# Optimization experiments

Measured on AMD Instinct MI355X. Metric: run time of the kernel, lower is better.

Reference implementation:

```python
import jax, jax.numpy as jnp
import numpy as np

B, C, H, W = 16, 512, 32, 32
GROUPS = 8
EPS = 1e-5


def setup_inputs() -> dict:
    key = jax.random.key(0)
    ks = jax.random.split(key, 7)
    s = 1.0 / np.sqrt(C)
    return {
        "x": jax.random.normal(ks[0], (B, C, H, W), dtype=jnp.float32),
        "gamma": jnp.ones((C,), dtype=jnp.float32),
        "beta": jnp.zeros((C,), dtype=jnp.float32),
        "w_qkv": jax.random.normal(ks[1], (3 * C, C), dtype=jnp.float32) * s,
        "b_qkv": jnp.zeros((3 * C,), dtype=jnp.float32),
        "w_proj": jax.random.normal(ks[2], (C, C), dtype=jnp.float32) * s,
        "b_proj": jnp.zeros((C,), dtype=jnp.float32),
    }


def group_norm(x, gamma, beta):
    b, c, h, w = x.shape
    xg = x.reshape(b, GROUPS, c // GROUPS, h, w)
    mean = xg.mean(axis=(2, 3, 4), keepdims=True)
    var = xg.var(axis=(2, 3, 4), keepdims=True)
    xn = ((xg - mean) * jax.lax.rsqrt(var + EPS)).reshape(b, c, h, w)
    return xn * gamma[None, :, None, None] + beta[None, :, None, None]


def reference(x, gamma, beta, w_qkv, b_qkv, w_proj, b_proj):
    b, c, h, w = x.shape
    n = h * w
    hn = group_norm(x, gamma, beta)
    # 1x1 conv == channel matmul: [3C, C] x [B, C, N] -> [B, 3C, N]
    qkv = jnp.einsum('oc,bcn->bon', w_qkv, hn.reshape(b, c, n)) + b_qkv[None, :, None]
    q, k, v = jnp.split(qkv, 3, axis=1)  # each [B, C, N]
    scale = c ** (-0.5)
    # scores [B, N, N]: q^T k
    attn = jax.nn.softmax(jnp.einsum('bcn,bcm->bnm', q, k) * scale, axis=-1)
    out = jnp.einsum('bnm,bcm->bcn', attn, v)  # [B, C, N]
    proj = jnp.einsum('oc,bcn->bon', w_proj, out) + b_proj[None, :, None]
    return x + proj.reshape(b, c, h, w)
```

## Files before the change

kernel.cpp:

```cpp
#include <hip/hip_runtime.h>


#define BATCH 16
#define CCH 512
#define NSP 1024
#define EPSV 1e-5f
#define BK 32

typedef short bf16x8 __attribute__((ext_vector_type(8)));
typedef float f32x4 __attribute__((ext_vector_type(4)));

__device__ __forceinline__ unsigned short f2bf(float f) {
    unsigned int u = __float_as_uint(f);
    u += 0x7FFF + ((u >> 16) & 1);
    return (unsigned short)(u >> 16);
}

__device__ __forceinline__ void glds16(const void* g, void* l) {
    __builtin_amdgcn_global_load_lds(
        (const __attribute__((address_space(1))) unsigned int*)g,
        (__attribute__((address_space(3))) unsigned int*)l, 16, 0, 0);
}

#define XCD_MAP(GX_LOG2, PER, xv, yv, bv)                 \
    const int lin_ = blockIdx.x;                          \
    const int xcd_ = lin_ & 7;                            \
    int slot_ = lin_ >> 3;                                \
    const int hi_ = (slot_ >= (PER)) ? 1 : 0;             \
    const int bv = xcd_ + 8 * hi_;                        \
    slot_ -= hi_ * (PER);                                 \
    const int xv = slot_ & ((1 << (GX_LOG2)) - 1);        \
    const int yv = slot_ >> (GX_LOG2);

__device__ __forceinline__ void gemm128_loop(
    const unsigned short* __restrict__ Ag, const unsigned short* __restrict__ Bg,
    int astr, int bstr, int ktot, short* Al, short* Bl, f32x4* acc) {
    const int t = threadIdx.x;
    const int w = t >> 6, lane = t & 63;
    const int wr = (w >> 1) * 64, wc = (w & 1) * 64;
    const int fr = lane & 15, fko = (lane >> 4) * 8;
    const int r0 = t >> 2;
    const int kc = (t & 3) * 8;
    short* Alb0 = Al + w * 512;
    short* Alb1 = Al + 2048 + w * 512;
    short* Blb0 = Bl + w * 512;
    short* Blb1 = Bl + 2048 + w * 512;
    for (int k0 = 0; k0 < ktot; k0 += BK) {
        glds16(Ag + (size_t)r0 * astr + k0 + kc, Alb0);
        glds16(Ag + (size_t)(r0 + 64) * astr + k0 + kc, Alb1);
        glds16(Bg + (size_t)r0 * bstr + k0 + kc, Blb0);
        glds16(Bg + (size_t)(r0 + 64) * bstr + k0 + kc, Blb1);
        __syncthreads();
        bf16x8 af[4], bfr[4];
#pragma unroll
        for (int mi = 0; mi < 4; mi++)
            af[mi] = *(const bf16x8*)(Al + (wr + mi * 16 + fr) * BK + fko);
#pragma unroll
        for (int ni = 0; ni < 4; ni++)
            bfr[ni] = *(const bf16x8*)(Bl + (wc + ni * 16 + fr) * BK + fko);
#pragma unroll
        for (int mi = 0; mi < 4; mi++)
#pragma unroll
            for (int ni = 0; ni < 4; ni++)
                acc[mi * 4 + ni] = __builtin_amdgcn_mfma_f32_16x16x32_bf16(
                    af[mi], bfr[ni], acc[mi * 4 + ni], 0, 0, 0);
        __syncthreads();
    }
}

#define EPI_SETUP()                                          \
    const int t = threadIdx.x, lane = t & 63, w = t >> 6;    \
    const int wr = (w >> 1) * 64, wc = (w & 1) * 64;         \
    const int fr = lane & 15, rr0 = (lane >> 4) * 4;

#define ACC_INIT(acc)                                        \
    f32x4 acc[16];                                           \
    _Pragma("unroll") for (int i = 0; i < 16; i++)           \
        acc[i] = (f32x4){0.f, 0.f, 0.f, 0.f};

__global__ __launch_bounds__(256) void setup_k(
    const float* __restrict__ x, float* __restrict__ stats,
    const float* __restrict__ wa, unsigned short* __restrict__ oa, int na4,
    const float* __restrict__ wb, unsigned short* __restrict__ ob, int nb4) {
    const int t = threadIdx.x;
    if (blockIdx.x < 128) {
        const int bg = blockIdx.x;
        const float4* xp = (const float4*)(x + (size_t)bg * 65536);
        float s = 0.f, q = 0.f;
#pragma unroll
        for (int i = 0; i < 64; i++) {
            float4 v = xp[t + i * 256];
            s += v.x + v.y + v.z + v.w;
            q += v.x * v.x + v.y * v.y + v.z * v.z + v.w * v.w;
        }
#pragma unroll
        for (int off = 32; off; off >>= 1) {
            s += __shfl_down(s, off);
            q += __shfl_down(q, off);
        }
        __shared__ float rs[4], rq[4];
        const int wave = t >> 6, lane = t & 63;
        if (lane == 0) { rs[wave] = s; rq[wave] = q; }
        __syncthreads();
        if (t == 0) {
            float S = rs[0] + rs[1] + rs[2] + rs[3];
            float Q = rq[0] + rq[1] + rq[2] + rq[3];
            const float inv = 1.f / 65536.f;
            float mean = S * inv;
            float var = Q * inv - mean * mean;
            stats[bg * 2] = mean;
            stats[bg * 2 + 1] = rsqrtf(var + EPSV);
        }
    } else {
        int i = (blockIdx.x - 128) * 256 + t;
        const float* src;
        unsigned short* dst;
        int j;
        if (i < na4) { src = wa; dst = oa; j = i; }
        else { j = i - na4; if (j >= nb4) return; src = wb; dst = ob; }
        float4 v = ((const float4*)src)[j];
        ushort4 o;
        o.x = f2bf(v.x); o.y = f2bf(v.y); o.z = f2bf(v.z); o.w = f2bf(v.w);
        ((ushort4*)dst)[j] = o;
    }
}

__global__ __launch_bounds__(256) void gn_tr_k(
    const float* __restrict__ x, const float* __restrict__ gamma,
    const float* __restrict__ beta, const float* __restrict__ stats,
    unsigned short* __restrict__ hn_t) {
    const int nt = blockIdx.x, ct = blockIdx.y, b = blockIdx.z;
    __shared__ __align__(16) unsigned short T[64 * 72];
    const int t = threadIdx.x;
    const float mean = stats[(b * 8 + ct) * 2];
    const float rstd = stats[(b * 8 + ct) * 2 + 1];
    const int cl = t >> 2, nc = t & 3;
    const int c = ct * 64 + cl;
    const float ga = gamma[c] * rstd;
    const float be = beta[c] - mean * ga;
    const float4* xp = (const float4*)(x + ((size_t)b * CCH + c) * NSP + nt * 64);
#pragma unroll
    for (int j = 0; j < 4; j++) {
        float4 v = xp[nc * 4 + j];
        int n = nc * 16 + j * 4;
        T[(n + 0) * 72 + cl] = f2bf(v.x * ga + be);
        T[(n + 1) * 72 + cl] = f2bf(v.y * ga + be);
        T[(n + 2) * 72 + cl] = f2bf(v.z * ga + be);
        T[(n + 3) * 72 + cl] = f2bf(v.w * ga + be);
    }
    __syncthreads();
    const int nl = t >> 2, cc = t & 3;
    unsigned short* dst = hn_t + ((size_t)b * NSP + nt * 64 + nl) * CCH + ct * 64 + cc * 16;
    const unsigned short* src = T + nl * 72 + cc * 16;
    *(uint4*)dst = *(const uint4*)src;
    *(uint4*)(dst + 8) = *(const uint4*)(src + 8);
}

__global__ __launch_bounds__(256) void gemm_qkv_k(
    const unsigned short* __restrict__ hn_t, const unsigned short* __restrict__ wq,
    const float* __restrict__ bq, unsigned short* __restrict__ QKt,
    unsigned short* __restrict__ Vb) {
    __shared__ __align__(16) short Al[128 * BK], Bl[128 * BK];
    XCD_MAP(3, 96, xb, y, b);
    const int ntc = xb * 128;
    ACC_INIT(acc);
    if (y < 8) {
        const int mt = y * 128;
        gemm128_loop(hn_t + ((size_t)b * NSP + mt) * CCH,
                     wq + (size_t)ntc * CCH, CCH, CCH, CCH, Al, Bl, acc);
        unsigned short* Ob = QKt + (size_t)b * NSP * 1024;
        EPI_SETUP();
#pragma unroll
        for (int ni = 0; ni < 4; ni++) {
            int col = ntc + wc + ni * 16 + fr;
            float bias = bq[col];
#pragma unroll
            for (int mi = 0; mi < 4; mi++) {
                int row = mt + wr + mi * 16 + rr0;
#pragma unroll
                for (int r = 0; r < 4; r++)
                    Ob[(size_t)(row + r) * 1024 + col] = f2bf(acc[mi * 4 + ni][r] + bias);
            }
        }
    } else {
        const int mt = (y - 8) * 128;
        gemm128_loop(wq + (size_t)(1024 + mt) * CCH,
                     hn_t + ((size_t)b * NSP + ntc) * CCH, CCH, CCH, CCH, Al, Bl, acc);
        unsigned short* Ob = Vb + (size_t)b * CCH * NSP;
        EPI_SETUP();
#pragma unroll
        for (int mi = 0; mi < 4; mi++) {
            int row = mt + wr + mi * 16 + rr0;
#pragma unroll
            for (int r = 0; r < 4; r++) {
                float bias = bq[1024 + row + r];
#pragma unroll
                for (int ni = 0; ni < 4; ni++) {
                    int col = ntc + wc + ni * 16 + fr;
                    Ob[(size_t)(row + r) * NSP + col] = f2bf(acc[mi * 4 + ni][r] + bias);
                }
            }
        }
    }
}

__global__ __launch_bounds__(256) void gemm_scores_k(
    const unsigned short* __restrict__ QKt, unsigned short* __restrict__ expS,
    float* __restrict__ Lsum) {
    __shared__ __align__(16) short Al[128 * BK], Bl[128 * BK];
    XCD_MAP(3, 64, xb, yb, b);
    const int nt = xb * 128, mt = yb * 128;
    const unsigned short* base = QKt + (size_t)b * NSP * 1024;
    ACC_INIT(acc);
    gemm128_loop(base + (size_t)mt * 1024, base + (size_t)nt * 1024 + 512,
                 1024, 1024, 512, Al, Bl, acc);
    unsigned short* Ob = expS + (size_t)b * NSP * NSP;
    float* Ls = Lsum + (size_t)b * NSP;
    const float scale = 0.044194173824159216f;
    EPI_SETUP();
#pragma unroll
    for (int mi = 0; mi < 4; mi++) {
#pragma unroll
        for (int r = 0; r < 4; r++) {
            const int row = mt + wr + mi * 16 + rr0 + r;
            float rs = 0.f;
#pragma unroll
            for (int ni = 0; ni < 4; ni++) {
                int col = nt + wc + ni * 16 + fr;
                float e = __expf(acc[mi * 4 + ni][r] * scale);
                Ob[(size_t)row * NSP + col] = f2bf(e);
                rs += e;
            }
            rs += __shfl_xor(rs, 1);
            rs += __shfl_xor(rs, 2);
            rs += __shfl_xor(rs, 4);
            rs += __shfl_xor(rs, 8);
            if (fr == 0) atomicAdd(&Ls[row], rs);
        }
    }
}

__global__ __launch_bounds__(256) void gemm_pv_k(
    const unsigned short* __restrict__ expS, const unsigned short* __restrict__ Vb,
    const float* __restrict__ Lsum, unsigned short* __restrict__ At) {
    __shared__ __align__(16) short Al[128 * BK], Bl[128 * BK];
    XCD_MAP(2, 32, xb, yb, b);
    const int ntc = xb * 128, mt = yb * 128;
    ACC_INIT(acc);
    gemm128_loop(expS + ((size_t)b * NSP + mt) * NSP,
                 Vb + ((size_t)b * CCH + ntc) * NSP, NSP, NSP, NSP, Al, Bl, acc);
    unsigned short* Ob = At + (size_t)b * NSP * CCH;
    const float* Ls = Lsum + (size_t)b * NSP;
    EPI_SETUP();
#pragma unroll
    for (int mi = 0; mi < 4; mi++) {
        int row = mt + wr + mi * 16 + rr0;
#pragma unroll
        for (int r = 0; r < 4; r++) {
            float inv = __builtin_amdgcn_rcpf(Ls[row + r]);
#pragma unroll
            for (int ni = 0; ni < 4; ni++) {
                int col = ntc + wc + ni * 16 + fr;
                Ob[(size_t)(row + r) * CCH + col] = f2bf(acc[mi * 4 + ni][r] * inv);
            }
        }
    }
}

__global__ __launch_bounds__(256) void gemm_proj_k(
    const unsigned short* __restrict__ At, const unsigned short* __restrict__ wp,
    const float* __restrict__ bp, const float* __restrict__ x,
    float* __restrict__ out) {
    __shared__ __align__(16) short Al[128 * BK], Bl[128 * BK];
    XCD_MAP(3, 32, xb, yb, b);
    const int nt = xb * 128, mt = yb * 128;
    ACC_INIT(acc);
    gemm128_loop(wp + (size_t)mt * CCH, At + ((size_t)b * NSP + nt) * CCH,
                 CCH, CCH, CCH, Al, Bl, acc);
    const size_t bbase = (size_t)b * CCH * NSP;
    EPI_SETUP();
#pragma unroll
    for (int mi = 0; mi < 4; mi++) {
        int row = mt + wr + mi * 16 + rr0;
#pragma unroll
        for (int r = 0; r < 4; r++) {
            float bias = bp[row + r];
#pragma unroll
            for (int ni = 0; ni < 4; ni++) {
                int col = nt + wc + ni * 16 + fr;
                size_t idx = bbase + (size_t)(row + r) * NSP + col;
                out[idx] = x[idx] + bias + acc[mi * 4 + ni][r];
            }
        }
    }
}

extern "C" void kernel_launch(void* const* d_in, const int* in_sizes, int n_in,
                              void* d_out, int out_size, void* d_ws, size_t ws_size,
                              hipStream_t stream) {
    const float* x = (const float*)d_in[0];
    const float* gamma = (const float*)d_in[1];
    const float* beta = (const float*)d_in[2];
    const float* w_qkv = (const float*)d_in[3];
    const float* b_qkv = (const float*)d_in[4];
    const float* w_proj = (const float*)d_in[5];
    const float* b_proj = (const float*)d_in[6];
    float* out = (float*)d_out;

    char* ws = (char*)d_ws;
    const size_t MB = 1048576;
    unsigned short* wqkv_bf = (unsigned short*)ws;
    unsigned short* wproj_bf = (unsigned short*)(ws + 1572864);
    float* stats = (float*)(ws + 2 * MB);
    float* Lsum = (float*)(ws + 2 * MB + 65536);
    unsigned short* hn_t = (unsigned short*)(ws + 4 * MB);
    unsigned short* At = hn_t;
    unsigned short* QKt = (unsigned short*)(ws + 24 * MB);
    unsigned short* Vb = (unsigned short*)(ws + 60 * MB);
    unsigned short* expS = (unsigned short*)(ws + 80 * MB);

    hipMemsetAsync(Lsum, 0, BATCH * NSP * sizeof(float), stream);
    setup_k<<<1152, 256, 0, stream>>>(x, stats, w_qkv, wqkv_bf, 196608,
                                      w_proj, wproj_bf, 65536);
    gn_tr_k<<<dim3(16, 8, BATCH), 256, 0, stream>>>(x, gamma, beta, stats, hn_t);
    gemm_qkv_k<<<1536, 256, 0, stream>>>(hn_t, wqkv_bf, b_qkv, QKt, Vb);
    gemm_scores_k<<<1024, 256, 0, stream>>>(QKt, expS, Lsum);
    gemm_pv_k<<<512, 256, 0, stream>>>(expS, Vb, Lsum, At);
    gemm_proj_k<<<512, 256, 0, stream>>>(At, wproj_bf, b_proj, x, out);
}
```

Before: 225.7 us.

## Double-buffer GEMM LDS tiles with register prefetch and fold Lsum memset into setup

Replaces the direct global-to-LDS loads in the shared GEMM loop with a register-staged, double-buffered pipeline. The next K tile is loaded into registers while MFMAs run on the current LDS buffer, then written to the other buffer, so each step needs one barrier instead of two. It also drops the separate hipMemsetAsync by zeroing Lsum in extra blocks of setup_k. The cost is double the LDS per block, which may lower occupancy, plus extra VGPRs and VALU/LDS store instructions compared with the direct-to-LDS loads.

```diff
diff --git a/kernel.cpp b/kernel.cpp
--- a/kernel.cpp
+++ b/kernel.cpp
@@ -6,6 +6,7 @@
 #define NSP 1024
 #define EPSV 1e-5f
 #define BK 32
+#define BUFSZ 4096
 
 typedef short bf16x8 __attribute__((ext_vector_type(8)));
 typedef float f32x4 __attribute__((ext_vector_type(4)));
@@ -14,12 +15,6 @@
     unsigned int u = __float_as_uint(f);
     u += 0x7FFF + ((u >> 16) & 1);
     return (unsigned short)(u >> 16);
-}
-
-__device__ __forceinline__ void glds16(const void* g, void* l) {
-    __builtin_amdgcn_global_load_lds(
-        (const __attribute__((address_space(1))) unsigned int*)g,
-        (__attribute__((address_space(3))) unsigned int*)l, 16, 0, 0);
 }
 
 #define XCD_MAP(GX_LOG2, PER, xv, yv, bv)                 \
@@ -41,31 +36,66 @@
     const int fr = lane & 15, fko = (lane >> 4) * 8;
     const int r0 = t >> 2;
     const int kc = (t & 3) * 8;
-    short* Alb0 = Al + w * 512;
-    short* Alb1 = Al + 2048 + w * 512;
-    short* Blb0 = Bl + w * 512;
-    short* Blb1 = Bl + 2048 + w * 512;
-    for (int k0 = 0; k0 < ktot; k0 += BK) {
-        glds16(Ag + (size_t)r0 * astr + k0 + kc, Alb0);
-        glds16(Ag + (size_t)(r0 + 64) * astr + k0 + kc, Alb1);
-        glds16(Bg + (size_t)r0 * bstr + k0 + kc, Blb0);
-        glds16(Bg + (size_t)(r0 + 64) * bstr + k0 + kc, Blb1);
-        __syncthreads();
+    const unsigned short* Ap0 = Ag + (size_t)r0 * astr + kc;
+    const unsigned short* Ap1 = Ag + (size_t)(r0 + 64) * astr + kc;
+    const unsigned short* Bp0 = Bg + (size_t)r0 * bstr + kc;
+    const unsigned short* Bp1 = Bg + (size_t)(r0 + 64) * bstr + kc;
+    const int wof0 = r0 * BK + kc;
+    const int wof1 = (r0 + 64) * BK + kc;
+    bf16x8 ra0 = *(const bf16x8*)Ap0;
+    bf16x8 ra1 = *(const bf16x8*)Ap1;
+    bf16x8 rb0 = *(const bf16x8*)Bp0;
+    bf16x8 rb1 = *(const bf16x8*)Bp1;
+    *(bf16x8*)(Al + wof0) = ra0;
+    *(bf16x8*)(Al + wof1) = ra1;
+    *(bf16x8*)(Bl + wof0) = rb0;
+    *(bf16x8*)(Bl + wof1) = rb1;
+    __syncthreads();
+    const int nk = ktot / BK;
+    int buf = 0;
+    for (int k = 0; k < nk - 1; k++) {
+        const int kof = (k + 1) * BK;
+        ra0 = *(const bf16x8*)(Ap0 + kof);
+        ra1 = *(const bf16x8*)(Ap1 + kof);
+        rb0 = *(const bf16x8*)(Bp0 + kof);
+        rb1 = *(const bf16x8*)(Bp1 + kof);
+        const short* Ab = Al + buf * BUFSZ;
+        const short* Bb = Bl + buf * BUFSZ;
         bf16x8 af[4], bfr[4];
 #pragma unroll
         for (int mi = 0; mi < 4; mi++)
-            af[mi] = *(const bf16x8*)(Al + (wr + mi * 16 + fr) * BK + fko);
+            af[mi] = *(const bf16x8*)(Ab + (wr + mi * 16 + fr) * BK + fko);
 #pragma unroll
         for (int ni = 0; ni < 4; ni++)
-            bfr[ni] = *(const bf16x8*)(Bl + (wc + ni * 16 + fr) * BK + fko);
+            bfr[ni] = *(const bf16x8*)(Bb + (wc + ni * 16 + fr) * BK + fko);
 #pragma unroll
         for (int mi = 0; mi < 4; mi++)
 #pragma unroll
             for (int ni = 0; ni < 4; ni++)
                 acc[mi * 4 + ni] = __builtin_amdgcn_mfma_f32_16x16x32_bf16(
                     af[mi], bfr[ni], acc[mi * 4 + ni], 0, 0, 0);
+        buf ^= 1;
+        *(bf16x8*)(Al + buf * BUFSZ + wof0) = ra0;
+        *(bf16x8*)(Al + buf * BUFSZ + wof1) = ra1;
+        *(bf16x8*)(Bl + buf * BUFSZ + wof0) = rb0;
+        *(bf16x8*)(Bl + buf * BUFSZ + wof1) = rb1;
         __syncthreads();
     }
+    const short* Ab = Al + buf * BUFSZ;
+    const short* Bb = Bl + buf * BUFSZ;
+    bf16x8 af[4], bfr[4];
+#pragma unroll
+    for (int mi = 0; mi < 4; mi++)
+        af[mi] = *(const bf16x8*)(Ab + (wr + mi * 16 + fr) * BK + fko);
+#pragma unroll
+    for (int ni = 0; ni < 4; ni++)
+        bfr[ni] = *(const bf16x8*)(Bb + (wc + ni * 16 + fr) * BK + fko);
+#pragma unroll
+    for (int mi = 0; mi < 4; mi++)
+#pragma unroll
+        for (int ni = 0; ni < 4; ni++)
+            acc[mi * 4 + ni] = __builtin_amdgcn_mfma_f32_16x16x32_bf16(
+                af[mi], bfr[ni], acc[mi * 4 + ni], 0, 0, 0);
 }
 
 #define EPI_SETUP()                                          \
@@ -81,7 +111,8 @@
 __global__ __launch_bounds__(256) void setup_k(
     const float* __restrict__ x, float* __restrict__ stats,
     const float* __restrict__ wa, unsigned short* __restrict__ oa, int na4,
-    const float* __restrict__ wb, unsigned short* __restrict__ ob, int nb4) {
+    const float* __restrict__ wb, unsigned short* __restrict__ ob, int nb4,
+    float* __restrict__ Lsum) {
     const int t = threadIdx.x;
     if (blockIdx.x < 128) {
         const int bg = blockIdx.x;
@@ -111,7 +142,7 @@
             stats[bg * 2] = mean;
             stats[bg * 2 + 1] = rsqrtf(var + EPSV);
         }
-    } else {
+    } else if (blockIdx.x < 1152) {
         int i = (blockIdx.x - 128) * 256 + t;
         const float* src;
         unsigned short* dst;
@@ -122,6 +153,9 @@
         ushort4 o;
         o.x = f2bf(v.x); o.y = f2bf(v.y); o.z = f2bf(v.z); o.w = f2bf(v.w);
         ((ushort4*)dst)[j] = o;
+    } else {
+        int i = (blockIdx.x - 1152) * 256 + t;
+        ((float4*)Lsum)[i] = (float4){0.f, 0.f, 0.f, 0.f};
     }
 }
 
@@ -160,7 +194,7 @@
     const unsigned short* __restrict__ hn_t, const unsigned short* __restrict__ wq,
     const float* __restrict__ bq, unsigned short* __restrict__ QKt,
     unsigned short* __restrict__ Vb) {
-    __shared__ __align__(16) short Al[128 * BK], Bl[128 * BK];
+    __shared__ __align__(16) short Al[2 * BUFSZ], Bl[2 * BUFSZ];
     XCD_MAP(3, 96, xb, y, b);
     const int ntc = xb * 128;
     ACC_INIT(acc);
@@ -207,7 +241,7 @@
 __global__ __launch_bounds__(256) void gemm_scores_k(
     const unsigned short* __restrict__ QKt, unsigned short* __restrict__ expS,
     float* __restrict__ Lsum) {
-    __shared__ __align__(16) short Al[128 * BK], Bl[128 * BK];
+    __shared__ __align__(16) short Al[2 * BUFSZ], Bl[2 * BUFSZ];
     XCD_MAP(3, 64, xb, yb, b);
     const int nt = xb * 128, mt = yb * 128;
     const unsigned short* base = QKt + (size_t)b * NSP * 1024;
@@ -243,7 +277,7 @@
 __global__ __launch_bounds__(256) void gemm_pv_k(
     const unsigned short* __restrict__ expS, const unsigned short* __restrict__ Vb,
     const float* __restrict__ Lsum, unsigned short* __restrict__ At) {
-    __shared__ __align__(16) short Al[128 * BK], Bl[128 * BK];
+    __shared__ __align__(16) short Al[2 * BUFSZ], Bl[2 * BUFSZ];
     XCD_MAP(2, 32, xb, yb, b);
     const int ntc = xb * 128, mt = yb * 128;
     ACC_INIT(acc);
@@ -271,7 +305,7 @@
     const unsigned short* __restrict__ At, const unsigned short* __restrict__ wp,
     const float* __restrict__ bp, const float* __restrict__ x,
     float* __restrict__ out) {
-    __shared__ __align__(16) short Al[128 * BK], Bl[128 * BK];
+    __shared__ __align__(16) short Al[2 * BUFSZ], Bl[2 * BUFSZ];
     XCD_MAP(3, 32, xb, yb, b);
     const int nt = xb * 128, mt = yb * 128;
     ACC_INIT(acc);
@@ -319,9 +353,8 @@
     unsigned short* Vb = (unsigned short*)(ws + 60 * MB);
     unsigned short* expS = (unsigned short*)(ws + 80 * MB);
 
-    hipMemsetAsync(Lsum, 0, BATCH * NSP * sizeof(float), stream);
-    setup_k<<<1152, 256, 0, stream>>>(x, stats, w_qkv, wqkv_bf, 196608,
-                                      w_proj, wproj_bf, 65536);
+    setup_k<<<1168, 256, 0, stream>>>(x, stats, w_qkv, wqkv_bf, 196608,
+                                      w_proj, wproj_bf, 65536, Lsum);
     gn_tr_k<<<dim3(16, 8, BATCH), 256, 0, stream>>>(x, gamma, beta, stats, hn_t);
     gemm_qkv_k<<<1536, 256, 0, stream>>>(hn_t, wqkv_bf, b_qkv, QKt, Vb);
     gemm_scores_k<<<1024, 256, 0, stream>>>(QKt, expS, Lsum);
```

New measurement: 231.2 us. +2.4%, slower.

## Double K-step per barrier in GEMM loop and fold Lsum zeroing into setup

Applied to the files above, without the earlier changes.

The shared GEMM main loop now loads two 32-wide K slices (64 total) into two LDS halves per iteration, so each pair of __syncthreads covers twice as much MFMA work. This halves the barrier count and lets more global-to-LDS loads be in flight at once, at the cost of double the LDS per block, which may lower occupancy. Separately, the hipMemsetAsync of Lsum is replaced by extra blocks in setup_k that zero it, removing one launch.

```diff
diff --git a/kernel.cpp b/kernel.cpp
--- a/kernel.cpp
+++ b/kernel.cpp
@@ -6,6 +6,7 @@
 #define NSP 1024
 #define EPSV 1e-5f
 #define BK 32
+#define HT 4096
 
 typedef short bf16x8 __attribute__((ext_vector_type(8)));
 typedef float f32x4 __attribute__((ext_vector_type(4)));
@@ -41,29 +42,40 @@
     const int fr = lane & 15, fko = (lane >> 4) * 8;
     const int r0 = t >> 2;
     const int kc = (t & 3) * 8;
-    short* Alb0 = Al + w * 512;
-    short* Alb1 = Al + 2048 + w * 512;
-    short* Blb0 = Bl + w * 512;
-    short* Blb1 = Bl + 2048 + w * 512;
-    for (int k0 = 0; k0 < ktot; k0 += BK) {
-        glds16(Ag + (size_t)r0 * astr + k0 + kc, Alb0);
-        glds16(Ag + (size_t)(r0 + 64) * astr + k0 + kc, Alb1);
-        glds16(Bg + (size_t)r0 * bstr + k0 + kc, Blb0);
-        glds16(Bg + (size_t)(r0 + 64) * bstr + k0 + kc, Blb1);
+    const unsigned short* Ap0 = Ag + (size_t)r0 * astr + kc;
+    const unsigned short* Ap1 = Ag + (size_t)(r0 + 64) * astr + kc;
+    const unsigned short* Bp0 = Bg + (size_t)r0 * bstr + kc;
+    const unsigned short* Bp1 = Bg + (size_t)(r0 + 64) * bstr + kc;
+    short* Alw = Al + w * 512;
+    short* Blw = Bl + w * 512;
+    for (int k0 = 0; k0 < ktot; k0 += 64) {
+        glds16(Ap0 + k0, Alw);
+        glds16(Ap1 + k0, Alw + 2048);
+        glds16(Ap0 + k0 + 32, Alw + HT);
+        glds16(Ap1 + k0 + 32, Alw + HT + 2048);
+        glds16(Bp0 + k0, Blw);
+        glds16(Bp1 + k0, Blw + 2048);
+        glds16(Bp0 + k0 + 32, Blw + HT);
+        glds16(Bp1 + k0 + 32, Blw + HT + 2048);
         __syncthreads();
-        bf16x8 af[4], bfr[4];
-#pragma unroll
-        for (int mi = 0; mi < 4; mi++)
-            af[mi] = *(const bf16x8*)(Al + (wr + mi * 16 + fr) * BK + fko);
-#pragma unroll
-        for (int ni = 0; ni < 4; ni++)
-            bfr[ni] = *(const bf16x8*)(Bl + (wc + ni * 16 + fr) * BK + fko);
-#pragma unroll
-        for (int mi = 0; mi < 4; mi++)
+#pragma unroll
+        for (int h = 0; h < 2; h++) {
+            const short* Ab = Al + h * HT;
+            const short* Bb = Bl + h * HT;
+            bf16x8 af[4], bfr[4];
+#pragma unroll
+            for (int mi = 0; mi < 4; mi++)
+                af[mi] = *(const bf16x8*)(Ab + (wr + mi * 16 + fr) * BK + fko);
 #pragma unroll
             for (int ni = 0; ni < 4; ni++)
-                acc[mi * 4 + ni] = __builtin_amdgcn_mfma_f32_16x16x32_bf16(
-                    af[mi], bfr[ni], acc[mi * 4 + ni], 0, 0, 0);
+                bfr[ni] = *(const bf16x8*)(Bb + (wc + ni * 16 + fr) * BK + fko);
+#pragma unroll
+            for (int mi = 0; mi < 4; mi++)
+#pragma unroll
+                for (int ni = 0; ni < 4; ni++)
+                    acc[mi * 4 + ni] = __builtin_amdgcn_mfma_f32_16x16x32_bf16(
+                        af[mi], bfr[ni], acc[mi * 4 + ni], 0, 0, 0);
+        }
         __syncthreads();
     }
 }
@@ -81,7 +93,8 @@
 __global__ __launch_bounds__(256) void setup_k(
     const float* __restrict__ x, float* __restrict__ stats,
     const float* __restrict__ wa, unsigned short* __restrict__ oa, int na4,
-    const float* __restrict__ wb, unsigned short* __restrict__ ob, int nb4) {
+    const float* __restrict__ wb, unsigned short* __restrict__ ob, int nb4,
+    float* __restrict__ Lsum) {
     const int t = threadIdx.x;
     if (blockIdx.x < 128) {
         const int bg = blockIdx.x;
@@ -111,7 +124,7 @@
             stats[bg * 2] = mean;
             stats[bg * 2 + 1] = rsqrtf(var + EPSV);
         }
-    } else {
+    } else if (blockIdx.x < 1152) {
         int i = (blockIdx.x - 128) * 256 + t;
         const float* src;
         unsigned short* dst;
@@ -122,6 +135,9 @@
         ushort4 o;
         o.x = f2bf(v.x); o.y = f2bf(v.y); o.z = f2bf(v.z); o.w = f2bf(v.w);
         ((ushort4*)dst)[j] = o;
+    } else {
+        int i = (blockIdx.x - 1152) * 256 + t;
+        ((float4*)Lsum)[i] = (float4){0.f, 0.f, 0.f, 0.f};
     }
 }
 
@@ -160,7 +176,7 @@
     const unsigned short* __restrict__ hn_t, const unsigned short* __restrict__ wq,
     const float* __restrict__ bq, unsigned short* __restrict__ QKt,
     unsigned short* __restrict__ Vb) {
-    __shared__ __align__(16) short Al[128 * BK], Bl[128 * BK];
+    __shared__ __align__(16) short Al[2 * HT], Bl[2 * HT];
     XCD_MAP(3, 96, xb, y, b);
     const int ntc = xb * 128;
     ACC_INIT(acc);
@@ -207,7 +223,7 @@
 __global__ __launch_bounds__(256) void gemm_scores_k(
     const unsigned short* __restrict__ QKt, unsigned short* __restrict__ expS,
     float* __restrict__ Lsum) {
-    __shared__ __align__(16) short Al[128 * BK], Bl[128 * BK];
+    __shared__ __align__(16) short Al[2 * HT], Bl[2 * HT];
     XCD_MAP(3, 64, xb, yb, b);
     const int nt = xb * 128, mt = yb * 128;
     const unsigned short* base = QKt + (size_t)b * NSP * 1024;
@@ -243,7 +259,7 @@
 __global__ __launch_bounds__(256) void gemm_pv_k(
     const unsigned short* __restrict__ expS, const unsigned short* __restrict__ Vb,
     const float* __restrict__ Lsum, unsigned short* __restrict__ At) {
-    __shared__ __align__(16) short Al[128 * BK], Bl[128 * BK];
+    __shared__ __align__(16) short Al[2 * HT], Bl[2 * HT];
     XCD_MAP(2, 32, xb, yb, b);
     const int ntc = xb * 128, mt = yb * 128;
     ACC_INIT(acc);
@@ -271,7 +287,7 @@
     const unsigned short* __restrict__ At, const unsigned short* __restrict__ wp,
     const float* __restrict__ bp, const float* __restrict__ x,
     float* __restrict__ out) {
-    __shared__ __align__(16) short Al[128 * BK], Bl[128 * BK];
+    __shared__ __align__(16) short Al[2 * HT], Bl[2 * HT];
     XCD_MAP(3, 32, xb, yb, b);
     const int nt = xb * 128, mt = yb * 128;
     ACC_INIT(acc);
@@ -319,9 +335,8 @@
     unsigned short* Vb = (unsigned short*)(ws + 60 * MB);
     unsigned short* expS = (unsigned short*)(ws + 80 * MB);
 
-    hipMemsetAsync(Lsum, 0, BATCH * NSP * sizeof(float), stream);
-    setup_k<<<1152, 256, 0, stream>>>(x, stats, w_qkv, wqkv_bf, 196608,
-                                      w_proj, wproj_bf, 65536);
+    setup_k<<<1168, 256, 0, stream>>>(x, stats, w_qkv, wqkv_bf, 196608,
+                                      w_proj, wproj_bf, 65536, Lsum);
     gn_tr_k<<<dim3(16, 8, BATCH), 256, 0, stream>>>(x, gamma, beta, stats, hn_t);
     gemm_qkv_k<<<1536, 256, 0, stream>>>(hn_t, wqkv_bf, b_qkv, QKt, Vb);
     gemm_scores_k<<<1024, 256, 0, stream>>>(QKt, expS, Lsum);
```

After: 209.8 us. -7.0%, faster.
